# Kernel tuning notes

Measured on AMD Instinct MI355X. Metric: run time of the kernel, lower is better.

## Reference

```python
import jax, jax.numpy as jnp
import numpy as np

N_NODES = 100000
N_EDGES = 3200000
IN_DIM, BIG, HID = 4, 32, 2
EPS = 1e-5


def _lin_init(key, fan_in, fan_out):
    # torch nn.Linear default: U(-1/sqrt(fan_in), 1/sqrt(fan_in))
    kw, kb = jax.random.split(key)
    bound = 1.0 / np.sqrt(fan_in)
    w = jax.random.uniform(kw, (fan_in, fan_out), minval=-bound, maxval=bound, dtype=jnp.float32)
    b = jax.random.uniform(kb, (fan_out,), minval=-bound, maxval=bound, dtype=jnp.float32)
    return w, b


def setup_inputs() -> dict:
    key = jax.random.key(0)
    ks = jax.random.split(key, 9)
    x = jax.random.normal(ks[0], (N_NODES, IN_DIM), dtype=jnp.float32)
    edge_index = jax.random.randint(ks[1], (2, N_EDGES), 0, N_NODES, dtype=jnp.int32)
    bn_w = jnp.ones((IN_DIM,), jnp.float32)
    bn_b = jnp.zeros((IN_DIM,), jnp.float32)
    enc_w1, enc_b1 = _lin_init(ks[2], 2 * IN_DIM, BIG)
    enc_w2, enc_b2 = _lin_init(ks[3], BIG, BIG)
    enc_w3, enc_b3 = _lin_init(ks[4], BIG, HID)
    dec_w1, dec_b1 = _lin_init(ks[5], 2 * HID, BIG)
    dec_w2, dec_b2 = _lin_init(ks[6], BIG, BIG)
    dec_w3, dec_b3 = _lin_init(ks[7], BIG, IN_DIM)
    return dict(x=x, edge_index=edge_index, bn_w=bn_w, bn_b=bn_b,
                enc_w1=enc_w1, enc_b1=enc_b1, enc_w2=enc_w2, enc_b2=enc_b2,
                enc_w3=enc_w3, enc_b3=enc_b3,
                dec_w1=dec_w1, dec_b1=dec_b1, dec_w2=dec_w2, dec_b2=dec_b2,
                dec_w3=dec_w3, dec_b3=dec_b3)


def _edge_conv(x, src, dst, w1, b1, w2, b2, w3, b3, final_relu):
    # PyG EdgeConv: message = nn(cat([x_i, x_j - x_i])), mean-aggregated at target i (=dst)
    xi = x[dst]                     # [E, F] gather (target)
    xj = x[src]                     # [E, F] gather (source)
    h = jnp.concatenate([xi, xj - xi], axis=-1)  # [E, 2F]
    h = jax.nn.relu(h @ w1 + b1)
    h = jax.nn.relu(h @ w2 + b2)
    h = h @ w3 + b3
    if final_relu:
        h = jax.nn.relu(h)
    n = x.shape[0]
    agg = jax.ops.segment_sum(h, dst, num_segments=n)          # [N, out]
    cnt = jax.ops.segment_sum(jnp.ones((h.shape[0],), h.dtype), dst, num_segments=n)
    return agg / jnp.maximum(cnt, 1.0)[:, None]


def reference(x, edge_index, bn_w, bn_b,
              enc_w1, enc_b1, enc_w2, enc_b2, enc_w3, enc_b3,
              dec_w1, dec_b1, dec_w2, dec_b2, dec_w3, dec_b3):
    # BatchNorm1d (training mode: batch statistics, biased variance)
    mu = jnp.mean(x, axis=0)
    var = jnp.var(x, axis=0)
    h = (x - mu) * jax.lax.rsqrt(var + EPS) * bn_w + bn_b
    src, dst = edge_index[0], edge_index[1]
    h = _edge_conv(h, src, dst, enc_w1, enc_b1, enc_w2, enc_b2, enc_w3, enc_b3, final_relu=True)
    h = _edge_conv(h, src, dst, dec_w1, dec_b1, dec_w2, dec_b2, dec_w3, dec_b3, final_relu=False)
    return h
```

## Files before the change

### kernel.cpp

```cpp
#include <hip/hip_runtime.h>

#define N_NODES 100000
#define N_EDGES 3200000
#define EPS 1e-5f
#define NODE_BLOCKS 391
#define NB 782
#define BSTRIDE 4608
#define NSUB 3
#define S1_EPB 8192
#define S1_BLOCKS 391

typedef unsigned int uint;
typedef uint u32x4 __attribute__((ext_vector_type(4)));
typedef _Float16 f16x8 __attribute__((ext_vector_type(8)));
typedef float f32x16 __attribute__((ext_vector_type(16)));

static __device__ __forceinline__ f16x8 as_h8(u32x4 u) { return __builtin_bit_cast(f16x8, u); }
static __device__ __forceinline__ uint pkh(float a, float b) {
    return __builtin_bit_cast(uint, __builtin_amdgcn_cvt_pkrtz(a, b));
}
static __device__ __forceinline__ void swap32(uint& a, uint& b) {
    asm volatile("v_permlane32_swap_b32 %0, %1" : "+v"(a), "+v"(b));
}
static __device__ __forceinline__ uint prelu(uint u, uint z) {
    uint r;
    asm("v_pk_max_f16 %0, %1, %2" : "=v"(r) : "v"(u), "v"(z));
    return r;
}

#define MFMA(A, B, C) __builtin_amdgcn_mfma_f32_32x32x16_f16(as_h8(A), as_h8(B), (C), 0, 0, 0)

static __device__ __forceinline__ void repack(const f32x16& c, u32x4& f0, u32x4& f1, uint z) {
    uint p0 = prelu(pkh(c[0], c[1]), z),   p1 = prelu(pkh(c[2], c[3]), z);
    uint q0 = prelu(pkh(c[4], c[5]), z),   q1 = prelu(pkh(c[6], c[7]), z);
    uint p2 = prelu(pkh(c[8], c[9]), z),   p3 = prelu(pkh(c[10], c[11]), z);
    uint q2 = prelu(pkh(c[12], c[13]), z), q3 = prelu(pkh(c[14], c[15]), z);
    swap32(p0, q0); swap32(p1, q1);
    swap32(p2, q2); swap32(p3, q3);
    f0.x = p0; f0.y = p1; f0.z = q0; f0.w = q1;
    f1.x = p2; f1.y = p3; f1.z = q2; f1.w = q3;
}

static __device__ __forceinline__ void decode4(const int4& q, int* ss, int* ia) {
    int e0 = q.x, e1 = q.y, e2 = q.z, e3 = q.w;
    ss[0] = e0 & 0x1FFFF; ia[0] = (e0 >> 17) & 127;
    ss[1] = e1 & 0x1FFFF; ia[1] = (e1 >> 17) & 127;
    ss[2] = e2 & 0x1FFFF; ia[2] = (e2 >> 17) & 127;
    ss[3] = e3 & 0x1FFFF; ia[3] = (e3 >> 17) & 127;
    #pragma unroll
    for (int k = 0; k < 4; k++)
        if (ss[k] >= N_NODES) ss[k] = 0;
}

#define OFF_STATS  0
#define OFF_BCNT   1024
#define OFF_INVCNT 5120
#define OFF_AGG1   405120
#define OFF_DECW   1205120
#define OFF_BUCKET 1214848
#define OFF_PENC   15629696
#define OFF_PCNT   22836608
#define OFF_PDEC   26440064
#define OFF_ENCW   26440064


__global__ __launch_bounds__(256) void k_bn_stats(const float* __restrict__ x,
                                                  double* __restrict__ stats) {
    int i = blockIdx.x * 256 + threadIdx.x;
    float4 v = make_float4(0.f, 0.f, 0.f, 0.f);
    if (i < N_NODES) v = ((const float4*)x)[i];
    double a[8];
    a[0] = v.x; a[1] = v.y; a[2] = v.z; a[3] = v.w;
    a[4] = (double)v.x * v.x; a[5] = (double)v.y * v.y;
    a[6] = (double)v.z * v.z; a[7] = (double)v.w * v.w;
    #pragma unroll
    for (int off = 32; off > 0; off >>= 1) {
        #pragma unroll
        for (int j = 0; j < 8; j++) a[j] += __shfl_down(a[j], off);
    }
    __shared__ double smem[4][8];
    int wave = threadIdx.x >> 6;
    int lane = threadIdx.x & 63;
    if (lane == 0) {
        #pragma unroll
        for (int j = 0; j < 8; j++) smem[wave][j] = a[j];
    }
    __syncthreads();
    if (threadIdx.x == 0) {
        #pragma unroll
        for (int j = 0; j < 8; j++) {
            double t = smem[0][j] + smem[1][j] + smem[2][j] + smem[3][j];
            atomicAdd(&stats[j], t);
        }
    }
}

static __device__ __forceinline__ uint pk_part(float a, float b, int part) {
    _Float16 ah = (_Float16)a, bh = (_Float16)b;
    if (part) {
        a -= (float)ah; b -= (float)bh;
        ah = (_Float16)a; bh = (_Float16)b;
    }
    return (uint)__builtin_bit_cast(unsigned short, ah) |
           ((uint)__builtin_bit_cast(unsigned short, bh) << 16);
}

__global__ __launch_bounds__(256) void k_prep(const double* __restrict__ stats,
                                              const float* __restrict__ bn_w,
                                              const float* __restrict__ bn_b,
                                              const float* __restrict__ ew1,
                                              const float* __restrict__ eb1,
                                              const float* __restrict__ ew2,
                                              const float* __restrict__ eb2,
                                              const float* __restrict__ ew3,
                                              const float* __restrict__ eb3,
                                              const float* __restrict__ dw1,
                                              const float* __restrict__ db1,
                                              const float* __restrict__ dw2,
                                              const float* __restrict__ db2,
                                              const float* __restrict__ dw3,
                                              const float* __restrict__ db3,
                                              uint* __restrict__ encw,
                                              uint* __restrict__ decw) {
    int t = threadIdx.x;
    int lane = t >> 2, d = t & 3;
    int hi = lane >> 5, m = lane & 31;

    const double inv_n = 1.0 / (double)N_NODES;
    float sc[4], sh[4];
    #pragma unroll
    for (int dd = 0; dd < 4; dd++) {
        double mu = stats[dd] * inv_n;
        double vr = stats[4 + dd] * inv_n - mu * mu;
        float rs = (float)(1.0 / sqrt(vr + (double)EPS));
        sc[dd] = rs * bn_w[dd];
        sh[dd] = bn_b[dd] - (float)mu * sc[dd];
    }

    {
        int j = 2 * d;
        float a = ew1[j * 32 + m] * sc[j & 3];
        float bb = ew1[(j + 1) * 32 + m] * sc[(j + 1) & 3];
        encw[t] = pk_part(a, bb, hi);
    }
    {
        int j = 2 * d;
        float a = (j < 4) ? dw1[j * 32 + m] : 0.f;
        float bb = (j + 1 < 4) ? dw1[(j + 1) * 32 + m] : 0.f;
        decw[t] = pk_part(a, bb, hi);
    }
    #pragma unroll
    for (int tile = 0; tile < 2; tile++) {
        int k = 16 * tile + 8 * hi + 2 * d;
        {
            float a = ew2[k * 32 + m], bb = ew2[(k + 1) * 32 + m];
            encw[256 + tile * 256 + t] = pk_part(a, bb, 0);
            encw[768 + tile * 256 + t] = pk_part(a, bb, 1);
        }
        {
            float a = dw2[k * 32 + m], bb = dw2[(k + 1) * 32 + m];
            decw[256 + tile * 256 + t] = pk_part(a, bb, 0);
            decw[768 + tile * 256 + t] = pk_part(a, bb, 1);
        }
        {
            float a = 0.f, bb = 0.f;
            if (m == 0 || m == 4) {
                int o = m >> 2;
                a = ew3[k * 2 + o]; bb = ew3[(k + 1) * 2 + o];
            }
            encw[1280 + tile * 256 + t] = pk_part(a, bb, 0);
        }
        {
            float a = 0.f, bb = 0.f;
            if ((m & 3) < 2 && m < 6) {
                int o = (m & 1) + 2 * (m >> 2);
                a = dw3[k * 4 + o]; bb = dw3[(k + 1) * 4 + o];
            }
            decw[1280 + tile * 256 + t] = pk_part(a, bb, 0);
        }
    }
    if (t < 32) {
        int hh = t >> 4, r = t & 15;
        int row = (r & 3) + 8 * (r >> 2) + 4 * hh;
        float b1p = eb1[row];
        #pragma unroll
        for (int dd = 0; dd < 4; dd++) b1p += ew1[dd * 32 + row] * sh[dd];
        ((float*)encw)[1792 + t] = b1p;
        ((float*)encw)[1824 + t] = eb2[row];
        ((float*)encw)[1856 + t] = (row == 0) ? eb3[0] : (row == 4) ? eb3[1] : 0.f;
        ((float*)decw)[1792 + t] = db1[row];
        ((float*)decw)[1824 + t] = db2[row];
        ((float*)decw)[1856 + t] =
            ((row & 3) < 2 && row < 6) ? db3[(row & 1) + 2 * (row >> 2)] : 0.f;
    }
}

__global__ __launch_bounds__(256) void k_s1(const int* __restrict__ ei,
                                            int* __restrict__ bcnt,
                                            int* __restrict__ bucket_buf) {
    __shared__ int hist[NB];
    __shared__ int base[NB];
    __shared__ int run[NB];
    __shared__ int gbase[NB];
    __shared__ int entries[S1_EPB];
    __shared__ unsigned short bk16[S1_EPB];
    __shared__ int wsum[4];
    int tid = threadIdx.x;
    int e0 = blockIdx.x * S1_EPB;
    for (int i = tid; i < NB; i += 256) hist[i] = 0;
    __syncthreads();
    #pragma unroll
    for (int k = 0; k < 32; k++) {
        int e = e0 + k * 256 + tid;
        if (e < N_EDGES) atomicAdd(&hist[ei[N_EDGES + e] >> 7], 1);
    }
    __syncthreads();
    int t4 = tid * 4;
    int h0 = (t4 + 0 < NB) ? hist[t4 + 0] : 0;
    int h1 = (t4 + 1 < NB) ? hist[t4 + 1] : 0;
    int h2 = (t4 + 2 < NB) ? hist[t4 + 2] : 0;
    int h3 = (t4 + 3 < NB) ? hist[t4 + 3] : 0;
    int tsum = h0 + h1 + h2 + h3;
    int lane = tid & 63, wv = tid >> 6;
    int xs = tsum;
    #pragma unroll
    for (int off = 1; off < 64; off <<= 1) {
        int u = __shfl_up(xs, off);
        if (lane >= off) xs += u;
    }
    if (lane == 63) wsum[wv] = xs;
    __syncthreads();
    int wo = 0;
    #pragma unroll
    for (int w = 0; w < 4; w++) if (w < wv) wo += wsum[w];
    int texcl = wo + xs - tsum;
    if (t4 + 0 < NB) base[t4 + 0] = texcl;
    if (t4 + 1 < NB) base[t4 + 1] = texcl + h0;
    if (t4 + 2 < NB) base[t4 + 2] = texcl + h0 + h1;
    if (t4 + 3 < NB) base[t4 + 3] = texcl + h0 + h1 + h2;
    __syncthreads();
    for (int i = tid; i < NB; i += 256) {
        int h = hist[i];
        gbase[i] = i * BSTRIDE + (h ? atomicAdd(&bcnt[i], h) : 0);
        run[i] = base[i];
    }
    __syncthreads();
    #pragma unroll
    for (int k = 0; k < 32; k++) {
        int e = e0 + k * 256 + tid;
        if (e < N_EDGES) {
            int s = ei[e];
            int d = ei[N_EDGES + e];
            int b = d >> 7;
            int r = atomicAdd(&run[b], 1);
            entries[r] = s | ((d & 127) << 17);
            bk16[r] = (unsigned short)b;
        }
    }
    __syncthreads();
    int nloc = min(S1_EPB, N_EDGES - e0);
    for (int idx = tid; idx < nloc; idx += 256) {
        int b = bk16[idx];
        bucket_buf[gbase[b] + (idx - base[b])] = entries[idx];
    }
}

__global__ __launch_bounds__(256, 3) void k_enc_partial(const float* __restrict__ x,
                                                        const int* __restrict__ bucket_buf,
                                                        const int* __restrict__ bcnt,
                                                        float2* __restrict__ penc,
                                                        int* __restrict__ pcnt,
                                                        const uint* __restrict__ encw) {
    __shared__ float4 xs[128];
    __shared__ float acc0[128], acc1[128];
    __shared__ int lc[128];
    int b = blockIdx.x, sub = blockIdx.y, tid = threadIdx.x;
    int lane = tid & 63, hi = lane >> 5, col = lane & 31, wv = tid >> 6;
    int cb = bcnt[b];
    int node0 = b << 7;

    if (tid < 128) {
        acc0[tid] = 0.f; acc1[tid] = 0.f; lc[tid] = 0;
        int n = node0 + tid;
        if (n >= N_NODES) n = 0;
        xs[tid] = ((const float4*)x)[n];
    }
    __syncthreads();

    const u32x4* W4 = (const u32x4*)encw;
    u32x4 w1   = W4[lane];
    u32x4 w2h0 = W4[64 + lane],  w2h1 = W4[128 + lane];
    u32x4 w2l0 = W4[192 + lane], w2l1 = W4[256 + lane];
    u32x4 w30  = W4[320 + lane], w31  = W4[384 + lane];
    const float* tf = (const float*)encw;
    f32x16 b1f, b2f;
    {
        const float4* p1 = (const float4*)(tf + 1792 + hi * 16);
        const float4* p2 = (const float4*)(tf + 1824 + hi * 16);
        #pragma unroll
        for (int q = 0; q < 4; q++) {
            float4 a = p1[q], c = p2[q];
            b1f[4 * q] = a.x; b1f[4 * q + 1] = a.y; b1f[4 * q + 2] = a.z; b1f[4 * q + 3] = a.w;
            b2f[4 * q] = c.x; b2f[4 * q + 1] = c.y; b2f[4 * q + 2] = c.z; b2f[4 * q + 3] = c.w;
        }
    }
    float bc0 = tf[1856 + hi * 16] - b2f[0];
    float* accH = hi ? acc1 : acc0;
    uint z = 0;

    int wb0 = sub * 1536 + wv * 128;
    if (wb0 < cb) {
        const int4* BB = (const int4*)&bucket_buf[b * BSTRIDE];
        int i0 = (wb0 >> 2) + col;
        int4 qa = BB[i0];
        int4 qb = BB[i0 + 128];
        int4 qc = BB[i0 + 256];
        bool act1 = (wb0 + 512) < cb;
        bool act2 = (wb0 + 1024) < cb;

        auto enc_win = [&](const int* ia, const float4* xg, int wb) {
            #pragma unroll
            for (int j = 0; j < 4; j++) {
                float4 xi = xs[ia[j]];
                u32x4 xf;
                xf.x = pkh(xi.x, xi.y);
                xf.y = pkh(xi.z, xi.w);
                xf.z = pkh(xg[j].x - xi.x, xg[j].y - xi.y);
                xf.w = pkh(xg[j].z - xi.z, xg[j].w - xi.w);
                f32x16 c = MFMA(w1, xf, b1f);
                u32x4 f0, f1;
                repack(c, f0, f1, z);
                f32x16 c2 = MFMA(w2h0, f0, b2f);
                c2 = MFMA(w2h1, f1, c2);
                c2 = MFMA(w2l0, f0, c2);
                c2 = MFMA(w2l1, f1, c2);
                u32x4 e0, e1;
                repack(c2, e0, e1, z);
                f32x16 c3 = MFMA(w30, e0, b2f);
                c3 = MFMA(w31, e1, c3);
                float o = fmaxf(c3[0] + bc0, 0.f);
                if ((wb + col * 4 + j) < cb) {
                    atomicAdd(&accH[ia[j]], o);
                    if (hi == 0) atomicAdd(&lc[ia[j]], 1);
                }
            }
        };

        int s0[4], s1[4], s2[4], ia0[4], ia1[4], ia2[4];
        float4 xg0[4], xg1[4], xg2[4];
        decode4(qa, s0, ia0);
        #pragma unroll
        for (int k = 0; k < 4; k++) xg0[k] = ((const float4*)x)[s0[k]];
        if (act1) {
            decode4(qb, s1, ia1);
            #pragma unroll
            for (int k = 0; k < 4; k++) xg1[k] = ((const float4*)x)[s1[k]];
        }
        enc_win(ia0, xg0, wb0);
        if (act2) {
            decode4(qc, s2, ia2);
            #pragma unroll
            for (int k = 0; k < 4; k++) xg2[k] = ((const float4*)x)[s2[k]];
        }
        if (act1) enc_win(ia1, xg1, wb0 + 512);
        if (act2) enc_win(ia2, xg2, wb0 + 1024);
    }
    __syncthreads();
    if (tid < 128) {
        int pb = b * NSUB + sub;
        penc[pb * 128 + tid] = make_float2(acc0[tid], acc1[tid]);
        pcnt[pb * 128 + tid] = lc[tid];
    }
}

__global__ __launch_bounds__(256) void k_reduce_enc_p(const float2* __restrict__ penc,
                                                      const int* __restrict__ pcnt,
                                                      float2* __restrict__ agg1,
                                                      float* __restrict__ invcnt) {
    int i = blockIdx.x * 256 + threadIdx.x;
    if (i >= N_NODES) return;
    int b = i >> 7, l = i & 127;
    float a0 = 0.f, a1 = 0.f;
    int c = 0;
    #pragma unroll
    for (int sub = 0; sub < NSUB; sub++) {
        int idx = (b * NSUB + sub) * 128 + l;
        float2 p = penc[idx];
        a0 += p.x; a1 += p.y;
        c += pcnt[idx];
    }
    float ic = 1.0f / (float)(c > 1 ? c : 1);
    invcnt[i] = ic;
    agg1[i] = make_float2(a0 * ic, a1 * ic);
}

__global__ __launch_bounds__(256, 3) void k_dec_partial(const float2* __restrict__ henc,
                                                        const int* __restrict__ bucket_buf,
                                                        const int* __restrict__ bcnt,
                                                        float4* __restrict__ pdec,
                                                        const uint* __restrict__ decw) {
    __shared__ float2 hld[128];
    __shared__ float a0s[128], a1s[128], a2s[128], a3s[128];
    int b = blockIdx.x, sub = blockIdx.y, tid = threadIdx.x;
    int lane = tid & 63, hi = lane >> 5, col = lane & 31, wv = tid >> 6;
    int cb = bcnt[b];
    int node0 = b << 7;

    if (tid < 128) {
        a0s[tid] = 0.f; a1s[tid] = 0.f; a2s[tid] = 0.f; a3s[tid] = 0.f;
        int n = node0 + tid;
        if (n >= N_NODES) n = 0;
        hld[tid] = henc[n];
    }
    __syncthreads();

    const u32x4* W4 = (const u32x4*)decw;
    u32x4 v1   = W4[lane];
    u32x4 v2h0 = W4[64 + lane],  v2h1 = W4[128 + lane];
    u32x4 v2l0 = W4[192 + lane], v2l1 = W4[256 + lane];
    u32x4 w30  = W4[320 + lane], w31  = W4[384 + lane];
    const float* tf = (const float*)decw;
    f32x16 b1f, b2f;
    {
        const float4* p1 = (const float4*)(tf + 1792 + hi * 16);
        const float4* p2 = (const float4*)(tf + 1824 + hi * 16);
        #pragma unroll
        for (int q = 0; q < 4; q++) {
            float4 a = p1[q], c = p2[q];
            b1f[4 * q] = a.x; b1f[4 * q + 1] = a.y; b1f[4 * q + 2] = a.z; b1f[4 * q + 3] = a.w;
            b2f[4 * q] = c.x; b2f[4 * q + 1] = c.y; b2f[4 * q + 2] = c.z; b2f[4 * q + 3] = c.w;
        }
    }
    float bc0 = tf[1856 + hi * 16 + 0] - b2f[0];
    float bc1 = tf[1856 + hi * 16 + 1] - b2f[1];
    float* accA = hi ? a2s : a0s;
    float* accB = hi ? a3s : a1s;
    uint z = 0;

    int wb0 = sub * 1536 + wv * 128;
    if (wb0 < cb) {
        const int4* BB = (const int4*)&bucket_buf[b * BSTRIDE];
        int i0 = (wb0 >> 2) + col;
        int4 qa = BB[i0];
        int4 qb = BB[i0 + 128];
        int4 qc = BB[i0 + 256];
        bool act1 = (wb0 + 512) < cb;
        bool act2 = (wb0 + 1024) < cb;

        auto dec_win = [&](const int* ia, const float2* hj, int wb) {
            #pragma unroll
            for (int j = 0; j < 4; j++) {
                float2 h2 = hld[ia[j]];
                u32x4 xf;
                xf.x = pkh(h2.x, h2.y);
                xf.y = pkh(hj[j].x - h2.x, hj[j].y - h2.y);
                xf.z = 0u; xf.w = 0u;
                f32x16 c = MFMA(v1, xf, b1f);
                u32x4 f0, f1;
                repack(c, f0, f1, z);
                f32x16 c2 = MFMA(v2h0, f0, b2f);
                c2 = MFMA(v2h1, f1, c2);
                c2 = MFMA(v2l0, f0, c2);
                c2 = MFMA(v2l1, f1, c2);
                u32x4 e0, e1;
                repack(c2, e0, e1, z);
                f32x16 c3 = MFMA(w30, e0, b2f);
                c3 = MFMA(w31, e1, c3);
                float o0 = c3[0] + bc0;
                float o1 = c3[1] + bc1;
                if ((wb + col * 4 + j) < cb) {
                    atomicAdd(&accA[ia[j]], o0);
                    atomicAdd(&accB[ia[j]], o1);
                }
            }
        };

        int s0[4], s1[4], s2[4], ia0[4], ia1[4], ia2[4];
        float2 hg0[4], hg1[4], hg2[4];
        decode4(qa, s0, ia0);
        #pragma unroll
        for (int k = 0; k < 4; k++) hg0[k] = henc[s0[k]];
        if (act1) {
            decode4(qb, s1, ia1);
            #pragma unroll
            for (int k = 0; k < 4; k++) hg1[k] = henc[s1[k]];
        }
        dec_win(ia0, hg0, wb0);
        if (act2) {
            decode4(qc, s2, ia2);
            #pragma unroll
            for (int k = 0; k < 4; k++) hg2[k] = henc[s2[k]];
        }
        if (act1) dec_win(ia1, hg1, wb0 + 512);
        if (act2) dec_win(ia2, hg2, wb0 + 1024);
    }
    __syncthreads();
    if (tid < 128) {
        int pb = b * NSUB + sub;
        pdec[pb * 128 + tid] = make_float4(a0s[tid], a1s[tid], a2s[tid], a3s[tid]);
    }
}

__global__ __launch_bounds__(256) void k_reduce_dec_p(const float4* __restrict__ pdec,
                                                      const float* __restrict__ invcnt,
                                                      float4* __restrict__ out) {
    int i = blockIdx.x * 256 + threadIdx.x;
    if (i >= N_NODES) return;
    int b = i >> 7, l = i & 127;
    float a0 = 0.f, a1 = 0.f, a2 = 0.f, a3 = 0.f;
    #pragma unroll
    for (int sub = 0; sub < NSUB; sub++) {
        float4 p = pdec[(b * NSUB + sub) * 128 + l];
        a0 += p.x; a1 += p.y; a2 += p.z; a3 += p.w;
    }
    float ic = invcnt[i];
    out[i] = make_float4(a0 * ic, a1 * ic, a2 * ic, a3 * ic);
}

extern "C" void kernel_launch(void* const* d_in, const int* in_sizes, int n_in,
                              void* d_out, int out_size, void* d_ws, size_t ws_size,
                              hipStream_t stream) {
    const float* x    = (const float*)d_in[0];
    const int*   ei   = (const int*)d_in[1];
    const float* bn_w = (const float*)d_in[2];
    const float* bn_b = (const float*)d_in[3];
    const float* ew1  = (const float*)d_in[4];
    const float* eb1  = (const float*)d_in[5];
    const float* ew2  = (const float*)d_in[6];
    const float* eb2  = (const float*)d_in[7];
    const float* ew3  = (const float*)d_in[8];
    const float* eb3  = (const float*)d_in[9];
    const float* dw1  = (const float*)d_in[10];
    const float* db1  = (const float*)d_in[11];
    const float* dw2  = (const float*)d_in[12];
    const float* db2  = (const float*)d_in[13];
    const float* dw3  = (const float*)d_in[14];
    const float* db3  = (const float*)d_in[15];

    char* ws = (char*)d_ws;
    double* stats      = (double*)(ws + OFF_STATS);
    int*    bcnt       = (int*)(ws + OFF_BCNT);
    float*  invcnt     = (float*)(ws + OFF_INVCNT);
    float2* agg1       = (float2*)(ws + OFF_AGG1);
    uint*   decw       = (uint*)(ws + OFF_DECW);
    int*    bucket_buf = (int*)(ws + OFF_BUCKET);
    float2* penc       = (float2*)(ws + OFF_PENC);
    int*    pcnt       = (int*)(ws + OFF_PCNT);
    float4* pdec       = (float4*)(ws + OFF_PDEC);
    uint*   encw       = (uint*)(ws + OFF_ENCW);
    float4* out        = (float4*)d_out;

    hipMemsetAsync(ws, 0, 5120, stream);

    k_bn_stats<<<NODE_BLOCKS, 256, 0, stream>>>(x, stats);
    k_prep<<<1, 256, 0, stream>>>(stats, bn_w, bn_b, ew1, eb1, ew2, eb2, ew3, eb3,
                                  dw1, db1, dw2, db2, dw3, db3, encw, decw);
    k_s1<<<S1_BLOCKS, 256, 0, stream>>>(ei, bcnt, bucket_buf);
    k_enc_partial<<<dim3(NB, NSUB), 256, 0, stream>>>(x, bucket_buf, bcnt,
                                                      penc, pcnt, encw);
    k_reduce_enc_p<<<NODE_BLOCKS, 256, 0, stream>>>(penc, pcnt, agg1, invcnt);
    k_dec_partial<<<dim3(NB, NSUB), 256, 0, stream>>>(agg1, bucket_buf, bcnt, pdec, decw);
    k_reduce_dec_p<<<NODE_BLOCKS, 256, 0, stream>>>(pdec, invcnt, out);
}
```

Measured before the change: 305.4 us.

## Fold layer-1 bias into MFMA weights, halve gather lanes, raise occupancy

```diff
diff --git a/kernel.cpp b/kernel.cpp
--- a/kernel.cpp
+++ b/kernel.cpp
@@ -7,8 +7,8 @@
 #define NB 782
 #define BSTRIDE 4608
 #define NSUB 3
-#define S1_EPB 8192
-#define S1_BLOCKS 391
+#define S1_EPB 4096
+#define S1_BLOCKS 782
 
 typedef unsigned int uint;
 typedef uint u32x4 __attribute__((ext_vector_type(4)));
@@ -136,31 +136,36 @@
         sc[dd] = rs * bn_w[dd];
         sh[dd] = bn_b[dd] - (float)mu * sc[dd];
     }
-
+    float b1p = eb1[m];
+    #pragma unroll
+    for (int dd = 0; dd < 4; dd++) b1p += ew1[dd * 32 + m] * sh[dd];
+
+    int k0 = 8 * hi + 2 * d;
     {
-        int j = 2 * d;
-        float a = ew1[j * 32 + m] * sc[j & 3];
-        float bb = ew1[(j + 1) * 32 + m] * sc[(j + 1) & 3];
-        encw[t] = pk_part(a, bb, hi);
+        float v0 = (k0 < 8) ? ew1[k0 * 32 + m] * sc[k0 & 3]
+                            : (k0 == 8 ? b1p : 0.f);
+        float v1 = (k0 + 1 < 8) ? ew1[(k0 + 1) * 32 + m] * sc[(k0 + 1) & 3] : 0.f;
+        encw[t] = pk_part(v0, v1, 0);
+        encw[256 + t] = pk_part(v0, v1, 1);
     }
     {
-        int j = 2 * d;
-        float a = (j < 4) ? dw1[j * 32 + m] : 0.f;
-        float bb = (j + 1 < 4) ? dw1[(j + 1) * 32 + m] : 0.f;
-        decw[t] = pk_part(a, bb, hi);
+        float v0 = (k0 < 4) ? dw1[k0 * 32 + m] : (k0 == 4 ? db1[m] : 0.f);
+        float v1 = (k0 + 1 < 4) ? dw1[(k0 + 1) * 32 + m] : 0.f;
+        decw[t] = pk_part(v0, v1, 0);
+        decw[256 + t] = pk_part(v0, v1, 1);
     }
     #pragma unroll
     for (int tile = 0; tile < 2; tile++) {
-        int k = 16 * tile + 8 * hi + 2 * d;
+        int k = 16 * tile + k0;
         {
             float a = ew2[k * 32 + m], bb = ew2[(k + 1) * 32 + m];
-            encw[256 + tile * 256 + t] = pk_part(a, bb, 0);
-            encw[768 + tile * 256 + t] = pk_part(a, bb, 1);
+            encw[512 + tile * 256 + t] = pk_part(a, bb, 0);
+            encw[1024 + tile * 256 + t] = pk_part(a, bb, 1);
         }
         {
             float a = dw2[k * 32 + m], bb = dw2[(k + 1) * 32 + m];
-            decw[256 + tile * 256 + t] = pk_part(a, bb, 0);
-            decw[768 + tile * 256 + t] = pk_part(a, bb, 1);
+            decw[512 + tile * 256 + t] = pk_part(a, bb, 0);
+            decw[1024 + tile * 256 + t] = pk_part(a, bb, 1);
         }
         {
             float a = 0.f, bb = 0.f;
@@ -168,7 +173,7 @@
                 int o = m >> 2;
                 a = ew3[k * 2 + o]; bb = ew3[(k + 1) * 2 + o];
             }
-            encw[1280 + tile * 256 + t] = pk_part(a, bb, 0);
+            encw[1536 + tile * 256 + t] = pk_part(a, bb, 0);
         }
         {
             float a = 0.f, bb = 0.f;
@@ -176,21 +181,16 @@
                 int o = (m & 1) + 2 * (m >> 2);
                 a = dw3[k * 4 + o]; bb = dw3[(k + 1) * 4 + o];
             }
-            decw[1280 + tile * 256 + t] = pk_part(a, bb, 0);
+            decw[1536 + tile * 256 + t] = pk_part(a, bb, 0);
         }
     }
     if (t < 32) {
         int hh = t >> 4, r = t & 15;
         int row = (r & 3) + 8 * (r >> 2) + 4 * hh;
-        float b1p = eb1[row];
-        #pragma unroll
-        for (int dd = 0; dd < 4; dd++) b1p += ew1[dd * 32 + row] * sh[dd];
-        ((float*)encw)[1792 + t] = b1p;
-        ((float*)encw)[1824 + t] = eb2[row];
-        ((float*)encw)[1856 + t] = (row == 0) ? eb3[0] : (row == 4) ? eb3[1] : 0.f;
-        ((float*)decw)[1792 + t] = db1[row];
-        ((float*)decw)[1824 + t] = db2[row];
-        ((float*)decw)[1856 + t] =
+        ((float*)encw)[2048 + t] = eb2[row];
+        ((float*)encw)[2080 + t] = (row == 0) ? eb3[0] : (row == 4) ? eb3[1] : 0.f;
+        ((float*)decw)[2048 + t] = db2[row];
+        ((float*)decw)[2080 + t] =
             ((row & 3) < 2 && row < 6) ? db3[(row & 1) + 2 * (row >> 2)] : 0.f;
     }
 }
@@ -210,7 +210,7 @@
     for (int i = tid; i < NB; i += 256) hist[i] = 0;
     __syncthreads();
     #pragma unroll
-    for (int k = 0; k < 32; k++) {
+    for (int k = 0; k < S1_EPB / 256; k++) {
         int e = e0 + k * 256 + tid;
         if (e < N_EDGES) atomicAdd(&hist[ei[N_EDGES + e] >> 7], 1);
     }
@@ -246,7 +246,7 @@
     }
     __syncthreads();
     #pragma unroll
-    for (int k = 0; k < 32; k++) {
+    for (int k = 0; k < S1_EPB / 256; k++) {
         int e = e0 + k * 256 + tid;
         if (e < N_EDGES) {
             int s = ei[e];
@@ -265,7 +265,7 @@
     }
 }
 
-__global__ __launch_bounds__(256, 3) void k_enc_partial(const float* __restrict__ x,
+__global__ __launch_bounds__(256, 4) void k_enc_partial(const float* __restrict__ x,
                                                         const int* __restrict__ bucket_buf,
                                                         const int* __restrict__ bcnt,
                                                         float2* __restrict__ penc,
@@ -288,23 +288,21 @@
     __syncthreads();
 
     const u32x4* W4 = (const u32x4*)encw;
-    u32x4 w1   = W4[lane];
-    u32x4 w2h0 = W4[64 + lane],  w2h1 = W4[128 + lane];
-    u32x4 w2l0 = W4[192 + lane], w2l1 = W4[256 + lane];
-    u32x4 w30  = W4[320 + lane], w31  = W4[384 + lane];
+    u32x4 w1h  = W4[lane],       w1l  = W4[64 + lane];
+    u32x4 w2h0 = W4[128 + lane], w2h1 = W4[192 + lane];
+    u32x4 w2l0 = W4[256 + lane], w2l1 = W4[320 + lane];
+    u32x4 w30  = W4[384 + lane], w31  = W4[448 + lane];
     const float* tf = (const float*)encw;
-    f32x16 b1f, b2f;
+    f32x16 b2f;
     {
-        const float4* p1 = (const float4*)(tf + 1792 + hi * 16);
-        const float4* p2 = (const float4*)(tf + 1824 + hi * 16);
+        const float4* p2 = (const float4*)(tf + 2048 + hi * 16);
         #pragma unroll
         for (int q = 0; q < 4; q++) {
-            float4 a = p1[q], c = p2[q];
-            b1f[4 * q] = a.x; b1f[4 * q + 1] = a.y; b1f[4 * q + 2] = a.z; b1f[4 * q + 3] = a.w;
+            float4 c = p2[q];
             b2f[4 * q] = c.x; b2f[4 * q + 1] = c.y; b2f[4 * q + 2] = c.z; b2f[4 * q + 3] = c.w;
         }
     }
-    float bc0 = tf[1856 + hi * 16] - b2f[0];
+    float bc0 = tf[2080 + hi * 16] - b2f[0];
     float* accH = hi ? acc1 : acc0;
     uint z = 0;
 
@@ -321,13 +319,20 @@
         auto enc_win = [&](const int* ia, const float4* xg, int wb) {
             #pragma unroll
             for (int j = 0; j < 4; j++) {
-                float4 xi = xs[ia[j]];
                 u32x4 xf;
-                xf.x = pkh(xi.x, xi.y);
-                xf.y = pkh(xi.z, xi.w);
-                xf.z = pkh(xg[j].x - xi.x, xg[j].y - xi.y);
-                xf.w = pkh(xg[j].z - xi.z, xg[j].w - xi.w);
-                f32x16 c = MFMA(w1, xf, b1f);
+                if (hi == 0) {
+                    float4 xi = xs[ia[j]];
+                    xf.x = pkh(xi.x, xi.y);
+                    xf.y = pkh(xi.z, xi.w);
+                    xf.z = pkh(xg[j].x - xi.x, xg[j].y - xi.y);
+                    xf.w = pkh(xg[j].z - xi.z, xg[j].w - xi.w);
+                } else {
+                    xf.x = 0x00003C00u;
+                    xf.y = 0u; xf.z = 0u; xf.w = 0u;
+                }
+                f32x16 c = {};
+                c = MFMA(w1h, xf, c);
+                c = MFMA(w1l, xf, c);
                 u32x4 f0, f1;
                 repack(c, f0, f1, z);
                 f32x16 c2 = MFMA(w2h0, f0, b2f);
@@ -349,18 +354,24 @@
         int s0[4], s1[4], s2[4], ia0[4], ia1[4], ia2[4];
         float4 xg0[4], xg1[4], xg2[4];
         decode4(qa, s0, ia0);
-        #pragma unroll
-        for (int k = 0; k < 4; k++) xg0[k] = ((const float4*)x)[s0[k]];
+        if (hi == 0) {
+            #pragma unroll
+            for (int k = 0; k < 4; k++) xg0[k] = ((const float4*)x)[s0[k]];
+        }
         if (act1) {
             decode4(qb, s1, ia1);
-            #pragma unroll
-            for (int k = 0; k < 4; k++) xg1[k] = ((const float4*)x)[s1[k]];
+            if (hi == 0) {
+                #pragma unroll
+                for (int k = 0; k < 4; k++) xg1[k] = ((const float4*)x)[s1[k]];
+            }
         }
         enc_win(ia0, xg0, wb0);
         if (act2) {
             decode4(qc, s2, ia2);
-            #pragma unroll
-            for (int k = 0; k < 4; k++) xg2[k] = ((const float4*)x)[s2[k]];
+            if (hi == 0) {
+                #pragma unroll
+                for (int k = 0; k < 4; k++) xg2[k] = ((const float4*)x)[s2[k]];
+            }
         }
         if (act1) enc_win(ia1, xg1, wb0 + 512);
         if (act2) enc_win(ia2, xg2, wb0 + 1024);
@@ -394,7 +405,7 @@
     agg1[i] = make_float2(a0 * ic, a1 * ic);
 }
 
-__global__ __launch_bounds__(256, 3) void k_dec_partial(const float2* __restrict__ henc,
+__global__ __launch_bounds__(256, 4) void k_dec_partial(const float2* __restrict__ henc,
                                                         const int* __restrict__ bucket_buf,
                                                         const int* __restrict__ bcnt,
                                                         float4* __restrict__ pdec,
@@ -415,24 +426,22 @@
     __syncthreads();
 
     const u32x4* W4 = (const u32x4*)decw;
-    u32x4 v1   = W4[lane];
-    u32x4 v2h0 = W4[64 + lane],  v2h1 = W4[128 + lane];
-    u32x4 v2l0 = W4[192 + lane], v2l1 = W4[256 + lane];
-    u32x4 w30  = W4[320 + lane], w31  = W4[384 + lane];
+    u32x4 w1h  = W4[lane],       w1l  = W4[64 + lane];
+    u32x4 v2h0 = W4[128 + lane], v2h1 = W4[192 + lane];
+    u32x4 v2l0 = W4[256 + lane], v2l1 = W4[320 + lane];
+    u32x4 w30  = W4[384 + lane], w31  = W4[448 + lane];
     const float* tf = (const float*)decw;
-    f32x16 b1f, b2f;
+    f32x16 b2f;
     {
-        const float4* p1 = (const float4*)(tf + 1792 + hi * 16);
-        const float4* p2 = (const float4*)(tf + 1824 + hi * 16);
+        const float4* p2 = (const float4*)(tf + 2048 + hi * 16);
         #pragma unroll
         for (int q = 0; q < 4; q++) {
-            float4 a = p1[q], c = p2[q];
-            b1f[4 * q] = a.x; b1f[4 * q + 1] = a.y; b1f[4 * q + 2] = a.z; b1f[4 * q + 3] = a.w;
+            float4 c = p2[q];
             b2f[4 * q] = c.x; b2f[4 * q + 1] = c.y; b2f[4 * q + 2] = c.z; b2f[4 * q + 3] = c.w;
         }
     }
-    float bc0 = tf[1856 + hi * 16 + 0] - b2f[0];
-    float bc1 = tf[1856 + hi * 16 + 1] - b2f[1];
+    float bc0 = tf[2080 + hi * 16 + 0] - b2f[0];
+    float bc1 = tf[2080 + hi * 16 + 1] - b2f[1];
     float* accA = hi ? a2s : a0s;
     float* accB = hi ? a3s : a1s;
     uint z = 0;
@@ -450,12 +459,19 @@
         auto dec_win = [&](const int* ia, const float2* hj, int wb) {
             #pragma unroll
             for (int j = 0; j < 4; j++) {
-                float2 h2 = hld[ia[j]];
                 u32x4 xf;
-                xf.x = pkh(h2.x, h2.y);
-                xf.y = pkh(hj[j].x - h2.x, hj[j].y - h2.y);
-                xf.z = 0u; xf.w = 0u;
-                f32x16 c = MFMA(v1, xf, b1f);
+                if (hi == 0) {
+                    float2 h2 = hld[ia[j]];
+                    xf.x = pkh(h2.x, h2.y);
+                    xf.y = pkh(hj[j].x - h2.x, hj[j].y - h2.y);
+                    xf.z = 0x00003C00u;
+                    xf.w = 0u;
+                } else {
+                    xf.x = 0u; xf.y = 0u; xf.z = 0u; xf.w = 0u;
+                }
+                f32x16 c = {};
+                c = MFMA(w1h, xf, c);
+                c = MFMA(w1l, xf, c);
                 u32x4 f0, f1;
                 repack(c, f0, f1, z);
                 f32x16 c2 = MFMA(v2h0, f0, b2f);
@@ -478,18 +494,24 @@
         int s0[4], s1[4], s2[4], ia0[4], ia1[4], ia2[4];
         float2 hg0[4], hg1[4], hg2[4];
         decode4(qa, s0, ia0);
-        #pragma unroll
-        for (int k = 0; k < 4; k++) hg0[k] = henc[s0[k]];
+        if (hi == 0) {
+            #pragma unroll
+            for (int k = 0; k < 4; k++) hg0[k] = henc[s0[k]];
+        }
         if (act1) {
             decode4(qb, s1, ia1);
-            #pragma unroll
-            for (int k = 0; k < 4; k++) hg1[k] = henc[s1[k]];
+            if (hi == 0) {
+                #pragma unroll
+                for (int k = 0; k < 4; k++) hg1[k] = henc[s1[k]];
+            }
         }
         dec_win(ia0, hg0, wb0);
         if (act2) {
             decode4(qc, s2, ia2);
-            #pragma unroll
-            for (int k = 0; k < 4; k++) hg2[k] = henc[s2[k]];
+            if (hi == 0) {
+                #pragma unroll
+                for (int k = 0; k < 4; k++) hg2[k] = henc[s2[k]];
+            }
         }
         if (act1) dec_win(ia1, hg1, wb0 + 512);
         if (act2) dec_win(ia2, hg2, wb0 + 1024);
```

After: 310.9 us. About the same (+1.8%).
